# Performance work log

Hardware: AMD Instinct MI355X
Metric: run time of the kernel (lower is better)

The kernel has to match this reference:

```python
import jax, jax.numpy as jnp
import numpy as np

D_MODEL, D_K, D_V = 512, 64, 64


def setup_inputs() -> dict:
    key = jax.random.key(0)
    ks = jax.random.split(key, 9)
    b, n = 8, 4096
    scale = 1.0 / np.sqrt(D_MODEL)
    return {
        "q": jax.random.normal(ks[0], (b, n, D_MODEL), jnp.float32),
        "k": jax.random.normal(ks[1], (b, n, D_MODEL), jnp.float32),
        "v": jax.random.normal(ks[2], (b, n, D_MODEL), jnp.float32),
        "Wq": jax.random.normal(ks[3], (D_MODEL, D_K), jnp.float32) * scale,
        "bq": jnp.zeros((D_K,), jnp.float32),
        "Wk": jax.random.normal(ks[4], (D_MODEL, D_K), jnp.float32) * scale,
        "bk": jnp.zeros((D_K,), jnp.float32),
        "Wv": jax.random.normal(ks[5], (D_MODEL, D_V), jnp.float32) * scale,
        "bv": jnp.zeros((D_V,), jnp.float32),
        "mask": 0,
    }


def reference(q, k, v, Wq, bq, Wk, bk, Wv, bv, mask):
    # linear projections (torch Linear: x @ W^T + b; here W stored as [in,out])
    qp = jnp.einsum("bnd,de->bne", q, Wq) + bq  # (b,n,d_k)
    kp = jnp.einsum("bnd,de->bne", k, Wk) + bk  # (b,n,d_k)
    vp = jnp.einsum("bnd,de->bne", v, Wv) + bv  # (b,n,d_v)
    temper = D_K ** 0.5
    attn = jnp.einsum("bqe,bke->bqk", qp, kp) / temper  # (b,n,n)
    # original: attn[attn == mask] = -inf (equality mask on scores)
    attn = jnp.where(attn == jnp.float32(mask), -jnp.inf, attn)
    # NOTE: original's `attn.masked_fill(look_ahead_mask==0, -inf)` is NOT
    # in-place and its result is discarded, so look_ahead_mask has no effect.
    attn = jax.nn.softmax(attn, axis=-1)
    return jnp.einsum("bqk,bkv->bqv", attn, vp)  # (b,n,d_v)
```

## Files before the change

kernel.cpp:

```cpp
#include <hip/hip_runtime.h>

typedef _Float16 f16;
typedef _Float16 f16x2 __attribute__((ext_vector_type(2)));
typedef _Float16 f16x4 __attribute__((ext_vector_type(4)));
typedef _Float16 f16x8 __attribute__((ext_vector_type(8)));
typedef __fp16   h16x2 __attribute__((ext_vector_type(2)));
typedef float    f32x4 __attribute__((ext_vector_type(4)));
typedef float    f32x16 __attribute__((ext_vector_type(16)));

static constexpr float L2E = 1.44269504088896340736f;
static constexpr float QSC = 0.18033688011112042f;

static __device__ __forceinline__ f32x4 mfma16(f16x8 a, f16x8 b, f32x4 c) {
    return __builtin_amdgcn_mfma_f32_16x16x32_f16(a, b, c, 0, 0, 0);
}
static __device__ __forceinline__ f32x16 mfma32(f16x8 a, f16x8 b, f32x16 c) {
    return __builtin_amdgcn_mfma_f32_32x32x16_f16(a, b, c, 0, 0, 0);
}
static __device__ __forceinline__ f16x2 cvt_pk(float a, float b) {
    h16x2 t = __builtin_amdgcn_cvt_pkrtz(a, b);
    return __builtin_bit_cast(f16x2, t);
}
static __device__ __forceinline__ void gload16(const void* g, void* l) {
    __builtin_amdgcn_global_load_lds(
        (const __attribute__((address_space(1))) unsigned int*)g,
        (__attribute__((address_space(3))) unsigned int*)l, 16, 0, 0);
}

__global__ void ah_wt_prep(const float* __restrict__ Wq,
                           const float* __restrict__ Wk,
                           const float* __restrict__ Wv,
                           f16* __restrict__ WT) {
    const float* W = (blockIdx.x == 0) ? Wq : (blockIdx.x == 1) ? Wk : Wv;
    f16* o = WT + (size_t)blockIdx.x * (64 * 512);
    for (int i = threadIdx.x; i < 64 * 512; i += blockDim.x) {
        int col = i >> 9, e = i & 511;
        o[i] = (f16)W[e * 64 + col];
    }
}

__global__ __launch_bounds__(256, 2) void ah_proj(
    const float* __restrict__ Xq, const float* __restrict__ Xk, const float* __restrict__ Xv,
    const float* __restrict__ bq, const float* __restrict__ bk, const float* __restrict__ bv,
    const f16* __restrict__ WT,
    f16* __restrict__ qp, f16* __restrict__ kp, f16* __restrict__ vpT) {

    const int tens = blockIdx.y;
    const float* X    = (tens == 0) ? Xq : (tens == 1) ? Xk : Xv;
    const float* bias = (tens == 0) ? bq : (tens == 1) ? bk : bv;
    const f16* wt = WT + (size_t)tens * (64 * 512);
    const float osc = (tens == 0) ? QSC : 1.0f;

    const int lane = threadIdx.x & 63;
    const int wave = threadIdx.x >> 6;
    const int l15 = lane & 15, g = lane >> 4;
    const int row0 = blockIdx.x * 64;

    __shared__ __align__(16) f16 wlds[64 * 520];

    {
        int t = threadIdx.x;
        int row = t >> 2, q = t & 3;
        const f16* src = wt + (size_t)row * 512 + q * 128;
        f16* dst = &wlds[row * 520 + q * 128];
#pragma unroll
        for (int i = 0; i < 16; ++i)
            *(f16x8*)(dst + i * 8) = *(const f16x8*)(src + i * 8);
    }
    __syncthreads();

    f32x4 acc[4];
#pragma unroll
    for (int b = 0; b < 4; ++b) acc[b] = (f32x4){0.f, 0.f, 0.f, 0.f};

    const float* xrow = X + (size_t)(row0 + wave * 16 + l15) * 512;

#pragma unroll 4
    for (int ec = 0; ec < 16; ++ec) {
        const float* px = xrow + ec * 32 + g * 8;
        float4 v0 = *(const float4*)px;
        float4 v1 = *(const float4*)(px + 4);
        f16x2 p0 = cvt_pk(v0.x, v0.y), p1 = cvt_pk(v0.z, v0.w);
        f16x2 p2 = cvt_pk(v1.x, v1.y), p3 = cvt_pk(v1.z, v1.w);
        f16x8 a;
        a[0] = p0[0]; a[1] = p0[1]; a[2] = p1[0]; a[3] = p1[1];
        a[4] = p2[0]; a[5] = p2[1]; a[6] = p3[0]; a[7] = p3[1];
#pragma unroll
        for (int cf = 0; cf < 4; ++cf) {
            f16x8 bfr = *(const f16x8*)(&wlds[(cf * 16 + l15) * 520 + (ec * 4 + g) * 8]);
            acc[cf] = mfma16(a, bfr, acc[cf]);
        }
    }

    __syncthreads();

    f16* lds = wlds;
#pragma unroll
    for (int cf = 0; cf < 4; ++cf) {
        float b = bias[cf * 16 + l15];
#pragma unroll
        for (int r = 0; r < 4; ++r) {
            int rr = wave * 16 + g * 4 + r;
            lds[rr * 68 + cf * 16 + l15] = (f16)((acc[cf][r] + b) * osc);
        }
    }
    __syncthreads();

    if (tens < 2) {
        f16* o = ((tens == 0) ? qp : kp) + (size_t)row0 * 64;
        for (int c = threadIdx.x; c < 64 * 16; c += 256) {
            int r = c >> 4, ch = c & 15;
            *(f16x4*)(o + r * 64 + ch * 4) = *(const f16x4*)(&lds[r * 68 + ch * 4]);
        }
    } else {
        int b = row0 >> 12, n0 = row0 & 4095;
        f16* o = vpT + (size_t)b * 64 * 4096 + n0;
        for (int c = threadIdx.x; c < 64 * 16; c += 256) {
            int d = c >> 4, nch = c & 15;
            f16x4 v;
#pragma unroll
            for (int j = 0; j < 4; ++j) v[j] = lds[(nch * 4 + j) * 68 + d];
            *(f16x4*)(o + (size_t)d * 4096 + nch * 4) = v;
        }
    }
}

__global__ __launch_bounds__(512, 2) void ah_attn(
    const f16* __restrict__ qp, const f16* __restrict__ kp, const f16* __restrict__ vpT,
    const int* __restrict__ maskp, float* __restrict__ out) {

    const int id = blockIdx.x;
    const int batch = id & 7, qtile = id >> 3;
    const int lane = threadIdx.x & 63, wave = threadIdx.x >> 6;
    const int l31 = lane & 31, hi2 = lane >> 5;
    const int s = wave & 3, qg = wave >> 2;
    const int q0 = qtile * 128 + qg * 64;
    const float mthr = L2E * (float)maskp[0];

    const f16* qpb = qp + (size_t)batch * 4096 * 64;
    const f16* kpb = kp + (size_t)batch * 4096 * 64;
    const f16* vpb = vpT + (size_t)batch * 64 * 4096;

    __shared__ __align__(16) char smem[65536];
    __shared__ float mlx[2][4][2][32];

    const int krow = lane >> 3;
    const int vrow = lane >> 2;
    const int eswzK = (lane & 7) ^ krow;
    const int eswzV = (lane & 3) ^ (vrow & 3);
    const int swzK = l31 & 7, swzV = l31 & 3;

#define STAGE(DB, IT) do {                                                          \
    const int _k0 = (((IT) * 4 + s) << 5);                                          \
    char* _b = smem + ((s * 2 + (DB)) * 8192) + (qg ? 4096 : 0);                    \
    if (qg == 0) {                                                                  \
        _Pragma("unroll")                                                           \
        for (int _j = 0; _j < 4; ++_j)                                              \
            gload16(kpb + (size_t)(_k0 + _j * 8 + krow) * 64 + eswzK * 8,           \
                    _b + _j * 1024);                                                \
    } else {                                                                        \
        _Pragma("unroll")                                                           \
        for (int _j = 0; _j < 4; ++_j)                                              \
            gload16(vpb + (size_t)(_j * 16 + vrow) * 4096 + _k0 + eswzV * 8,        \
                    _b + _j * 1024);                                                \
    }                                                                               \
} while (0)

    f16x8 qf_[2][4];
#pragma unroll
    for (int qt = 0; qt < 2; ++qt)
#pragma unroll
        for (int st = 0; st < 4; ++st)
            qf_[qt][st] = *(const f16x8*)(qpb + (size_t)(q0 + qt * 32 + l31) * 64 + st * 16 + hi2 * 8);

    f32x16 oacc[2][2];
#pragma unroll
    for (int dt = 0; dt < 2; ++dt)
#pragma unroll
        for (int qt = 0; qt < 2; ++qt)
#pragma unroll
            for (int r = 0; r < 16; ++r) oacc[dt][qt][r] = 0.f;
    float ps[2] = {0.f, 0.f};

    STAGE(0, 0);
    int db = 0;
    for (int it = 0; it < 32; ++it) {
        if (it < 31) {
            STAGE(db ^ 1, it + 1);
            asm volatile("s_waitcnt vmcnt(4)" ::: "memory");
        } else {
            asm volatile("s_waitcnt vmcnt(0)" ::: "memory");
        }
        __builtin_amdgcn_s_barrier();
        __builtin_amdgcn_sched_barrier(0);

        const char* kb = smem + (s * 2 + db) * 8192;
        const char* vb = kb + 4096;

        f16x8 ka[4];
#pragma unroll
        for (int st = 0; st < 4; ++st)
            ka[st] = *(const f16x8*)(kb + l31 * 128 + (((st * 2 + hi2) ^ swzK) << 4));
        f32x16 sacc[2];
#pragma unroll
        for (int qt = 0; qt < 2; ++qt)
#pragma unroll
            for (int r = 0; r < 16; ++r) sacc[qt][r] = 0.f;
#pragma unroll
        for (int st = 0; st < 4; ++st)
#pragma unroll
            for (int qt = 0; qt < 2; ++qt)
                sacc[qt] = mfma32(ka[st], qf_[qt][st], sacc[qt]);

        f16x8 av[2][2];
#pragma unroll
        for (int dt = 0; dt < 2; ++dt)
#pragma unroll
            for (int t = 0; t < 2; ++t) {
                const char* p = vb + (dt * 32 + l31) * 64 + hi2 * 8;
                *(f16x4*)(&av[dt][t])       = *(const f16x4*)(p + (((t * 2 + 0) ^ swzV) << 4));
                *((f16x4*)(&av[dt][t]) + 1) = *(const f16x4*)(p + (((t * 2 + 1) ^ swzV) << 4));
            }

        f16x8 pb_[2][2];
#pragma unroll
        for (int qt = 0; qt < 2; ++qt)
#pragma unroll
            for (int t = 0; t < 2; ++t)
#pragma unroll
                for (int w = 0; w < 4; ++w) {
                    float s0 = sacc[qt][t * 8 + 2 * w];
                    float s1 = sacc[qt][t * 8 + 2 * w + 1];
                    float e0 = __builtin_amdgcn_exp2f(s0);
                    float e1 = __builtin_amdgcn_exp2f(s1);
                    float p0 = (s0 == mthr) ? 0.f : e0;
                    float p1 = (s1 == mthr) ? 0.f : e1;
                    ps[qt] += p0 + p1;
                    ((f16x2*)(&pb_[qt][t]))[w] = cvt_pk(p0, p1);
                }

#pragma unroll
        for (int dt = 0; dt < 2; ++dt)
#pragma unroll
            for (int qt = 0; qt < 2; ++qt)
#pragma unroll
                for (int t = 0; t < 2; ++t)
                    oacc[dt][qt] = mfma32(av[dt][t], pb_[qt][t], oacc[dt][qt]);

        __builtin_amdgcn_sched_barrier(0);
        __builtin_amdgcn_s_barrier();
        __builtin_amdgcn_sched_barrier(0);
        db ^= 1;
    }
#undef STAGE

    ps[0] += __shfl_xor(ps[0], 32);
    ps[1] += __shfl_xor(ps[1], 32);
    if (lane < 32) { mlx[qg][s][0][lane] = ps[0]; mlx[qg][s][1][lane] = ps[1]; }
    __syncthreads();

    float* SC = (float*)smem;
#define SCI(B, DT, QT, R) ((((qg * 2 + (B)) * 64) + ((DT) * 2 + (QT)) * 16 + (R)) * 64 + lane)
    if (s >= 2) {
#pragma unroll
        for (int dt = 0; dt < 2; ++dt)
#pragma unroll
            for (int qt = 0; qt < 2; ++qt)
#pragma unroll
                for (int r = 0; r < 16; ++r)
                    SC[SCI(s - 2, dt, qt, r)] = oacc[dt][qt][r];
    }
    __syncthreads();
    if (s < 2) {
#pragma unroll
        for (int dt = 0; dt < 2; ++dt)
#pragma unroll
            for (int qt = 0; qt < 2; ++qt)
#pragma unroll
                for (int r = 0; r < 16; ++r)
                    oacc[dt][qt][r] += SC[SCI(s, dt, qt, r)];
        if (s == 1) {
#pragma unroll
            for (int dt = 0; dt < 2; ++dt)
#pragma unroll
                for (int qt = 0; qt < 2; ++qt)
#pragma unroll
                    for (int r = 0; r < 16; ++r)
                        SC[SCI(1, dt, qt, r)] = oacc[dt][qt][r];
        }
    }
    __syncthreads();
    if (s == 0) {
        float inv[2];
#pragma unroll
        for (int qt = 0; qt < 2; ++qt)
            inv[qt] = 1.0f / (mlx[qg][0][qt][l31] + mlx[qg][1][qt][l31] +
                              mlx[qg][2][qt][l31] + mlx[qg][3][qt][l31]);
#pragma unroll
        for (int qt = 0; qt < 2; ++qt) {
            float* o0 = out + ((size_t)batch * 4096 + q0 + qt * 32 + l31) * 64;
#pragma unroll
            for (int dt = 0; dt < 2; ++dt)
#pragma unroll
                for (int rg = 0; rg < 4; ++rg) {
                    float4 v;
                    v.x = (oacc[dt][qt][rg * 4 + 0] + SC[SCI(1, dt, qt, rg * 4 + 0)]) * inv[qt];
                    v.y = (oacc[dt][qt][rg * 4 + 1] + SC[SCI(1, dt, qt, rg * 4 + 1)]) * inv[qt];
                    v.z = (oacc[dt][qt][rg * 4 + 2] + SC[SCI(1, dt, qt, rg * 4 + 2)]) * inv[qt];
                    v.w = (oacc[dt][qt][rg * 4 + 3] + SC[SCI(1, dt, qt, rg * 4 + 3)]) * inv[qt];
                    *(float4*)(o0 + dt * 32 + rg * 8 + hi2 * 4) = v;
                }
        }
    }
#undef SCI
}

extern "C" void kernel_launch(void* const* d_in, const int* in_sizes, int n_in,
                              void* d_out, int out_size, void* d_ws, size_t ws_size,
                              hipStream_t stream) {
    const float* q  = (const float*)d_in[0];
    const float* k  = (const float*)d_in[1];
    const float* v  = (const float*)d_in[2];
    const float* Wq = (const float*)d_in[3];
    const float* bq = (const float*)d_in[4];
    const float* Wk = (const float*)d_in[5];
    const float* bk = (const float*)d_in[6];
    const float* Wv = (const float*)d_in[7];
    const float* bv = (const float*)d_in[8];
    const int* mask = (const int*)d_in[9];
    float* out = (float*)d_out;

    const size_t NTOK = (size_t)8 * 4096;
    f16* qp  = (f16*)d_ws;
    f16* kp  = qp + NTOK * 64;
    f16* vpT = kp + NTOK * 64;
    f16* WT  = vpT + NTOK * 64;

    ah_wt_prep<<<dim3(3), 256, 0, stream>>>(Wq, Wk, Wv, WT);
    ah_proj<<<dim3(512, 3), 256, 0, stream>>>(q, k, v, bq, bk, bv, WT, qp, kp, vpT);
    ah_attn<<<dim3(256), 512, 0, stream>>>(qp, kp, vpT, mask, out);
}
```

Measured before the change: 127.1 us.

## Deepen attention K/V pipeline to four buffers and drop LDS weight staging in projection

The attention kernel moves from double-buffered to quad-buffered K/V staging in 128KB LDS with three tiles prefetched ahead, removing one barrier per iteration and changing the V tile LDS layout to an unswizzled chunked layout. The projection kernel uses smaller 128-thread blocks over 32 rows and reads weight fragments straight from global/L2 instead of copying them into LDS, which raises occupancy and removes the upfront LDS fill. Tradeoffs: the attention kernel is limited to one block per CU by LDS, the unswizzled V reads may cause bank conflicts, and weight reads now hit cache repeatedly.

```diff
diff --git a/kernel.cpp b/kernel.cpp
--- a/kernel.cpp
+++ b/kernel.cpp
@@ -39,7 +39,7 @@
     }
 }
 
-__global__ __launch_bounds__(256, 2) void ah_proj(
+__global__ __launch_bounds__(128, 8) void ah_proj(
     const float* __restrict__ Xq, const float* __restrict__ Xk, const float* __restrict__ Xv,
     const float* __restrict__ bq, const float* __restrict__ bk, const float* __restrict__ bv,
     const f16* __restrict__ WT,
@@ -54,26 +54,14 @@
     const int lane = threadIdx.x & 63;
     const int wave = threadIdx.x >> 6;
     const int l15 = lane & 15, g = lane >> 4;
-    const int row0 = blockIdx.x * 64;
-
-    __shared__ __align__(16) f16 wlds[64 * 520];
-
-    {
-        int t = threadIdx.x;
-        int row = t >> 2, q = t & 3;
-        const f16* src = wt + (size_t)row * 512 + q * 128;
-        f16* dst = &wlds[row * 520 + q * 128];
-#pragma unroll
-        for (int i = 0; i < 16; ++i)
-            *(f16x8*)(dst + i * 8) = *(const f16x8*)(src + i * 8);
-    }
-    __syncthreads();
+    const int row0 = blockIdx.x * 32;
+    const int wrow = wave * 16;
 
     f32x4 acc[4];
 #pragma unroll
     for (int b = 0; b < 4; ++b) acc[b] = (f32x4){0.f, 0.f, 0.f, 0.f};
 
-    const float* xrow = X + (size_t)(row0 + wave * 16 + l15) * 512;
+    const float* xrow = X + (size_t)(row0 + wrow + l15) * 512;
 
 #pragma unroll 4
     for (int ec = 0; ec < 16; ++ec) {
@@ -87,20 +75,18 @@
         a[4] = p2[0]; a[5] = p2[1]; a[6] = p3[0]; a[7] = p3[1];
 #pragma unroll
         for (int cf = 0; cf < 4; ++cf) {
-            f16x8 bfr = *(const f16x8*)(&wlds[(cf * 16 + l15) * 520 + (ec * 4 + g) * 8]);
+            f16x8 bfr = *(const f16x8*)(wt + (size_t)(cf * 16 + l15) * 512 + ec * 32 + g * 8);
             acc[cf] = mfma16(a, bfr, acc[cf]);
         }
     }
 
-    __syncthreads();
-
-    f16* lds = wlds;
+    __shared__ __align__(16) f16 lds[32 * 68];
 #pragma unroll
     for (int cf = 0; cf < 4; ++cf) {
         float b = bias[cf * 16 + l15];
 #pragma unroll
         for (int r = 0; r < 4; ++r) {
-            int rr = wave * 16 + g * 4 + r;
+            int rr = wrow + g * 4 + r;
             lds[rr * 68 + cf * 16 + l15] = (f16)((acc[cf][r] + b) * osc);
         }
     }
@@ -108,15 +94,15 @@
 
     if (tens < 2) {
         f16* o = ((tens == 0) ? qp : kp) + (size_t)row0 * 64;
-        for (int c = threadIdx.x; c < 64 * 16; c += 256) {
+        for (int c = threadIdx.x; c < 32 * 16; c += 128) {
             int r = c >> 4, ch = c & 15;
             *(f16x4*)(o + r * 64 + ch * 4) = *(const f16x4*)(&lds[r * 68 + ch * 4]);
         }
     } else {
         int b = row0 >> 12, n0 = row0 & 4095;
         f16* o = vpT + (size_t)b * 64 * 4096 + n0;
-        for (int c = threadIdx.x; c < 64 * 16; c += 256) {
-            int d = c >> 4, nch = c & 15;
+        for (int c = threadIdx.x; c < 64 * 8; c += 128) {
+            int d = c >> 3, nch = c & 7;
             f16x4 v;
 #pragma unroll
             for (int j = 0; j < 4; ++j) v[j] = lds[(nch * 4 + j) * 68 + d];
@@ -125,7 +111,7 @@
     }
 }
 
-__global__ __launch_bounds__(512, 2) void ah_attn(
+__global__ __launch_bounds__(512, 1) void ah_attn(
     const f16* __restrict__ qp, const f16* __restrict__ kp, const f16* __restrict__ vpT,
     const int* __restrict__ maskp, float* __restrict__ out) {
 
@@ -141,18 +127,16 @@
     const f16* kpb = kp + (size_t)batch * 4096 * 64;
     const f16* vpb = vpT + (size_t)batch * 64 * 4096;
 
-    __shared__ __align__(16) char smem[65536];
+    __shared__ __align__(16) char smem[131072];
     __shared__ float mlx[2][4][2][32];
 
     const int krow = lane >> 3;
-    const int vrow = lane >> 2;
     const int eswzK = (lane & 7) ^ krow;
-    const int eswzV = (lane & 3) ^ (vrow & 3);
-    const int swzK = l31 & 7, swzV = l31 & 3;
-
-#define STAGE(DB, IT) do {                                                          \
+    const int swzK = l31 & 7;
+
+#define STAGE(BUF, IT) do {                                                         \
     const int _k0 = (((IT) * 4 + s) << 5);                                          \
-    char* _b = smem + ((s * 2 + (DB)) * 8192) + (qg ? 4096 : 0);                    \
+    char* _b = smem + (s * 4 + (BUF)) * 8192 + (qg ? 4096 : 0);                     \
     if (qg == 0) {                                                                  \
         _Pragma("unroll")                                                           \
         for (int _j = 0; _j < 4; ++_j)                                              \
@@ -161,7 +145,8 @@
     } else {                                                                        \
         _Pragma("unroll")                                                           \
         for (int _j = 0; _j < 4; ++_j)                                              \
-            gload16(vpb + (size_t)(_j * 16 + vrow) * 4096 + _k0 + eswzV * 8,        \
+            gload16(vpb + (size_t)(_j * 16 + (lane & 15)) * 4096 + _k0 +            \
+                        (lane >> 4) * 8,                                            \
                     _b + _j * 1024);                                                \
     }                                                                               \
 } while (0)
@@ -182,19 +167,15 @@
             for (int r = 0; r < 16; ++r) oacc[dt][qt][r] = 0.f;
     float ps[2] = {0.f, 0.f};
 
-    STAGE(0, 0);
-    int db = 0;
+    STAGE(0, 0); STAGE(1, 1); STAGE(2, 2);
+    __builtin_amdgcn_s_barrier();
     for (int it = 0; it < 32; ++it) {
-        if (it < 31) {
-            STAGE(db ^ 1, it + 1);
-            asm volatile("s_waitcnt vmcnt(4)" ::: "memory");
-        } else {
-            asm volatile("s_waitcnt vmcnt(0)" ::: "memory");
-        }
-        __builtin_amdgcn_s_barrier();
+        if (it < 30)      asm volatile("s_waitcnt vmcnt(8)" ::: "memory");
+        else if (it == 30) asm volatile("s_waitcnt vmcnt(4)" ::: "memory");
+        else              asm volatile("s_waitcnt vmcnt(0)" ::: "memory");
         __builtin_amdgcn_sched_barrier(0);
 
-        const char* kb = smem + (s * 2 + db) * 8192;
+        const char* kb = smem + (s * 4 + (it & 3)) * 8192;
         const char* vb = kb + 4096;
 
         f16x8 ka[4];
@@ -214,13 +195,14 @@
 
         f16x8 av[2][2];
 #pragma unroll
-        for (int dt = 0; dt < 2; ++dt)
+        for (int dt = 0; dt < 2; ++dt) {
+            const char* vchunk = vb + (dt * 2 + (l31 >> 4)) * 1024 + (l31 & 15) * 16 + hi2 * 8;
 #pragma unroll
             for (int t = 0; t < 2; ++t) {
-                const char* p = vb + (dt * 32 + l31) * 64 + hi2 * 8;
-                *(f16x4*)(&av[dt][t])       = *(const f16x4*)(p + (((t * 2 + 0) ^ swzV) << 4));
-                *((f16x4*)(&av[dt][t]) + 1) = *(const f16x4*)(p + (((t * 2 + 1) ^ swzV) << 4));
+                *(f16x4*)(&av[dt][t])       = *(const f16x4*)(vchunk + (t * 2 + 0) * 256);
+                *((f16x4*)(&av[dt][t]) + 1) = *(const f16x4*)(vchunk + (t * 2 + 1) * 256);
             }
+        }
 
         f16x8 pb_[2][2];
 #pragma unroll
@@ -250,7 +232,7 @@
         __builtin_amdgcn_sched_barrier(0);
         __builtin_amdgcn_s_barrier();
         __builtin_amdgcn_sched_barrier(0);
-        db ^= 1;
+        if (it < 29) STAGE((it + 3) & 3, it + 3);
     }
 #undef STAGE
 
@@ -337,6 +319,6 @@
     f16* WT  = vpT + NTOK * 64;
 
     ah_wt_prep<<<dim3(3), 256, 0, stream>>>(Wq, Wk, Wv, WT);
-    ah_proj<<<dim3(512, 3), 256, 0, stream>>>(q, k, v, bq, bk, bv, WT, qp, kp, vpT);
+    ah_proj<<<dim3(1024, 3), 128, 0, stream>>>(q, k, v, bq, bk, bv, WT, qp, kp, vpT);
     ah_attn<<<dim3(256), 512, 0, stream>>>(qp, kp, vpT, mask, out);
 }
```

New measurement: 149.8 us. 1.18x slower.
